# Optimization experiments

Hardware: AMD Instinct MI355X
Metric: run time of the kernel (lower is better)

Reference implementation:

```python
import jax, jax.numpy as jnp
import numpy as np

B, S, D, H = 4, 2048, 1024, 16
DEPTH = D // H


def setup_inputs() -> dict:
    key = jax.random.key(0)
    ks = jax.random.split(key, 12)
    inp = {
        'v': jax.random.normal(ks[0], (B, S, D), dtype=jnp.float32),
        'k': jax.random.normal(ks[1], (B, S, D), dtype=jnp.float32),
        'q': jax.random.normal(ks[2], (B, S, D), dtype=jnp.float32),
        # key-padding mask: 1.0 = masked position, 0.0 = attend
        'mask': jax.random.randint(ks[3], (B, 1, 1, S), 0, 2).astype(jnp.float32),
        'Wq': jax.random.normal(ks[4], (D, D), dtype=jnp.float32) / np.sqrt(D),
        'bq': jnp.zeros((D,), dtype=jnp.float32),
        'Wk': jax.random.normal(ks[5], (D, D), dtype=jnp.float32) / np.sqrt(D),
        'bk': jnp.zeros((D,), dtype=jnp.float32),
        'Wv': jax.random.normal(ks[6], (D, D), dtype=jnp.float32) / np.sqrt(D),
        'bv': jnp.zeros((D,), dtype=jnp.float32),
        'Wo': jax.random.normal(ks[7], (D, D), dtype=jnp.float32) / np.sqrt(D),
        'bo': jnp.zeros((D,), dtype=jnp.float32),
    }
    return inp


def _split_heads(x):
    # [B, S, D] -> [B, H, S, depth]
    b, s, _ = x.shape
    return x.reshape(b, s, H, DEPTH).transpose(0, 2, 1, 3)


def reference(v, k, q, mask, Wq, bq, Wk, bk, Wv, bv, Wo, bo):
    qh = _split_heads(q @ Wq + bq)  # [B,H,S,depth]
    kh = _split_heads(k @ Wk + bk)
    vh = _split_heads(v @ Wv + bv)
    logits = jnp.einsum('bhqd,bhkd->bhqk', qh, kh) / jnp.sqrt(
        jnp.asarray(DEPTH, dtype=qh.dtype))
    logits = logits + mask * (-1e9)
    attn = jax.nn.softmax(logits, axis=-1)  # [B,H,Sq,Sk]
    out = jnp.einsum('bhqk,bhkd->bhqd', attn, vh)
    out = out.transpose(0, 2, 1, 3).reshape(q.shape[0], -1, D)  # [B,S,D]
    return out @ Wo + bo
```

## Files before the change

kernel.cpp:

```cpp
#include <hip/hip_runtime.h>
#include <hip/hip_bf16.h>
#include <stdint.h>


#define S_LEN 2048
#define NHEAD 16
#define DEPTH 64
#define DMODEL 1024

typedef __bf16 bf16x8 __attribute__((ext_vector_type(8)));
typedef float f32x4 __attribute__((ext_vector_type(4)));
typedef uint16_t u16x8 __attribute__((ext_vector_type(8)));
typedef uint16_t u16x4 __attribute__((ext_vector_type(4)));

#if __has_builtin(__builtin_amdgcn_exp2f)
#define EXP2F(x) __builtin_amdgcn_exp2f(x)
#else
#define EXP2F(x) __builtin_exp2f(x)
#endif

__device__ __forceinline__ uint16_t f2bf(float x) {
    __hip_bfloat16 h = __float2bfloat16(x);
    union { __hip_bfloat16 h; uint16_t u; } v; v.h = h; return v.u;
}
__device__ __forceinline__ u16x8 cvt8(const float* p) {
    f32x4 lo = *(const f32x4*)p, hi = *(const f32x4*)(p + 4);
    u16x8 r;
#pragma unroll
    for (int i = 0; i < 4; ++i) { r[i] = f2bf(lo[i]); r[i + 4] = f2bf(hi[i]); }
    return r;
}
__device__ __forceinline__ void async16(const void* g, void* l) {
    __builtin_amdgcn_global_load_lds((__attribute__((address_space(1))) void*)(g),
                                     (__attribute__((address_space(3))) void*)(l),
                                     16, 0, 0);
}

__global__ void mask_scan(const float* __restrict__ mask, int* __restrict__ gidx,
                          int* __restrict__ nb) {
    __shared__ int part[256];
    const int b = blockIdx.x, tid = threadIdx.x;
    int flags[8], cnt = 0;
#pragma unroll
    for (int i = 0; i < 8; ++i) {
        flags[i] = (mask[b * S_LEN + tid * 8 + i] == 0.0f) ? 1 : 0;
        cnt += flags[i];
    }
    part[tid] = cnt;
    __syncthreads();
    for (int st = 1; st < 256; st <<= 1) {
        int v = (tid >= st) ? part[tid - st] : 0;
        __syncthreads();
        part[tid] += v;
        __syncthreads();
    }
    int run = part[tid] - cnt;
#pragma unroll
    for (int i = 0; i < 8; ++i) {
        if (flags[i]) { gidx[b * S_LEN + run] = tid * 8 + i; ++run; }
    }
    if (tid == 255) nb[b] = part[255];
}

__global__ void transpose4(const float* __restrict__ w0, const float* __restrict__ w1,
                           const float* __restrict__ w2, const float* __restrict__ w3,
                           uint16_t* __restrict__ dst) {
    __shared__ uint16_t tile[32][33];
    const float* src = (blockIdx.z == 0) ? w0 : (blockIdx.z == 1) ? w1
                     : (blockIdx.z == 2) ? w2 : w3;
    uint16_t* d = dst + (size_t)blockIdx.z * DMODEL * DMODEL;
    int bx = blockIdx.x * 32, by = blockIdx.y * 32;
    int x = threadIdx.x, y0 = threadIdx.y;
#pragma unroll
    for (int i = 0; i < 4; ++i) {
        int y = y0 + i * 8;
        tile[y][x] = f2bf(src[(size_t)(by + y) * DMODEL + bx + x]);
    }
    __syncthreads();
#pragma unroll
    for (int i = 0; i < 4; ++i) {
        int y = y0 + i * 8;
        d[(size_t)(bx + y) * DMODEL + by + x] = tile[x][y];
    }
}

__global__ void cast2(const float* __restrict__ a, const float* __restrict__ b,
                      uint16_t* __restrict__ da, uint16_t* __restrict__ db) {
    const float* src = blockIdx.y ? b : a;
    uint16_t* dst = blockIdx.y ? db : da;
    size_t i = ((size_t)blockIdx.x * 256 + threadIdx.x) * 8;
    *(u16x8*)(dst + i) = cvt8(src + i);
}

__global__ void zero_tails(const int* __restrict__ nb, uint16_t* __restrict__ Kc,
                           uint16_t* __restrict__ Vc) {
    const int bh = blockIdx.x, b = bh >> 4, t = threadIdx.x;
    const int nbv = nb[b];
    const int end = ((nbv + 63) >> 6) << 6;
    const int tail = end - nbv;
    for (int i = t; i < tail * 64; i += 256) {
        int r = nbv + (i >> 6), c = i & 63;
        Kc[((size_t)bh * S_LEN + r) * DEPTH + c] = 0;
    }
    for (int i = t; i < tail * 64; i += 256) {
        int s = nbv + (i >> 6), d = i & 63;
        int off = s & 63;
        int c1 = ((off & 15) << 2) | (off >> 4);
        int c2 = ((((c1 >> 3) ^ (d & 7)) & 7) << 3) | (c1 & 7);
        Vc[((size_t)bh * DEPTH + d) * S_LEN + (s & ~63) + c2] = 0;
    }
}

__global__ __launch_bounds__(256, 2)
void qkv_gemm(const uint16_t* __restrict__ qb, const uint16_t* __restrict__ kb,
              const float* __restrict__ vf, const uint16_t* __restrict__ WT4,
              const float* __restrict__ bq, const float* __restrict__ bk,
              const float* __restrict__ bv, uint16_t* __restrict__ Qh,
              uint16_t* __restrict__ Kc, uint16_t* __restrict__ Vc,
              const int* __restrict__ gidx, const int* __restrict__ nb, int zbase) {
    const int z = zbase + blockIdx.z;
    const int fid = blockIdx.x + 8 * blockIdx.y;
    const int n0 = ((fid >> 3) & 7) * 128;
    const int m0 = ((((fid >> 6) << 3)) | (fid & 7)) * 128;
    const int b_ = m0 >> 11;
    int nbv = 0x7FFFFFFF;
    if (z >= 1) {
        nbv = nb[b_];
        if ((m0 & 2047) >= nbv) return;
    }

    __shared__ __align__(16) uint16_t As[128 * 32];
    __shared__ __align__(16) uint16_t Bs[128 * 32];

    const int t = threadIdx.x;
    const int lane = t & 63, quad = lane >> 4, l16 = lane & 15;
    const int w = t >> 6, wm = w >> 1, wn = w & 1;
    const int K = DMODEL;

    const int r_ld = lane >> 2;
    const int c_ld = (lane & 3) * 8;
    const uint16_t* gB = WT4 + (size_t)z * DMODEL * DMODEL + (size_t)(n0 + r_ld) * K + c_ld;
    const float* bias = (z == 0) ? bq : (z == 1) ? bk : bv;

    const int srow = t >> 1, scol = (t & 1) * 16;

    const uint16_t* pA0 = nullptr;
    const uint16_t* pA1 = nullptr;
    const float* Af32 = nullptr;
    if (z == 0) {
        pA0 = qb + (size_t)(m0 + (w * 2 + 0) * 16 + r_ld) * K + c_ld;
        pA1 = qb + (size_t)(m0 + (w * 2 + 1) * 16 + r_ld) * K + c_ld;
    } else if (z == 1) {
        int sp0 = (m0 & 2047) + (w * 2 + 0) * 16 + r_ld;
        int sp1 = sp0 + 16;
        int r0 = (sp0 < nbv) ? gidx[(b_ << 11) + sp0] : 0;
        int r1 = (sp1 < nbv) ? gidx[(b_ << 11) + sp1] : 0;
        pA0 = kb + ((size_t)(b_ << 11) + r0) * K + c_ld;
        pA1 = kb + ((size_t)(b_ << 11) + r1) * K + c_ld;
    } else {
        int sp = (m0 & 2047) + srow;
        int rs = (sp < nbv) ? gidx[(b_ << 11) + sp] : 0;
        Af32 = vf + ((size_t)(b_ << 11) + rs) * K + scol;
    }

    f32x4 acc[4][4];
    const f32x4 z4 = {0.f, 0.f, 0.f, 0.f};
#pragma unroll
    for (int mt = 0; mt < 4; ++mt)
#pragma unroll
        for (int nt = 0; nt < 4; ++nt) acc[mt][nt] = z4;

    for (int kc = 0; kc < K; kc += 32) {
#pragma unroll
        for (int i = 0; i < 2; ++i) {
            int c = w * 2 + i;
            async16(gB + (size_t)(c * 16) * K + kc, &Bs[c * 512]);
        }
        if (z <= 1) {
            async16(pA0 + kc, &As[(w * 2 + 0) * 512]);
            async16(pA1 + kc, &As[(w * 2 + 1) * 512]);
        } else {
            *(u16x8*)&As[srow * 32 + scol]     = cvt8(Af32 + kc);
            *(u16x8*)&As[srow * 32 + scol + 8] = cvt8(Af32 + kc + 8);
        }
        __syncthreads();

        bf16x8 af[4], bfr[4];
#pragma unroll
        for (int mt = 0; mt < 4; ++mt)
            af[mt] = *(const bf16x8*)&As[(wm * 64 + mt * 16 + l16) * 32 + quad * 8];
#pragma unroll
        for (int nt = 0; nt < 4; ++nt)
            bfr[nt] = *(const bf16x8*)&Bs[(wn * 64 + nt * 16 + l16) * 32 + quad * 8];
#pragma unroll
        for (int mt = 0; mt < 4; ++mt)
#pragma unroll
            for (int nt = 0; nt < 4; ++nt)
                acc[mt][nt] = __builtin_amdgcn_mfma_f32_16x16x32_bf16(af[mt], bfr[nt],
                                                                      acc[mt][nt], 0, 0, 0);
        __syncthreads();
    }

#pragma unroll
    for (int nt = 0; nt < 4; ++nt) {
        int col = n0 + wn * 64 + nt * 16 + l16;
        float bval = bias[col];
        int h = col >> 6, dp = col & 63;
#pragma unroll
        for (int mt = 0; mt < 4; ++mt) {
#pragma unroll
            for (int r = 0; r < 4; ++r) {
                int row = m0 + wm * 64 + mt * 16 + quad * 4 + r;
                float val = acc[mt][nt][r] + bval;
                int b = row >> 11, s = row & 2047;
                if (z == 0) {
                    Qh[(((size_t)(b * NHEAD + h)) * S_LEN + s) * DEPTH + dp] = f2bf(val);
                } else if (z == 1) {
                    if (s < nbv) {
                        int c2 = ((((dp >> 3) ^ (s & 7)) & 7) << 3) | (dp & 7);
                        Kc[(((size_t)(b * NHEAD + h)) * S_LEN + s) * DEPTH + c2] = f2bf(val);
                    }
                } else {
                    if (s < nbv) {
                        int off = s & 63;
                        int c1 = ((off & 15) << 2) | (off >> 4);
                        int c2 = ((((c1 >> 3) ^ (dp & 7)) & 7) << 3) | (c1 & 7);
                        Vc[(((size_t)(b * NHEAD + h)) * DEPTH + dp) * S_LEN
                           + (s & ~63) + c2] = f2bf(val);
                    }
                }
            }
        }
    }
}

__global__ __launch_bounds__(256, 2)
void out_gemm(const uint16_t* __restrict__ ctx, const uint16_t* __restrict__ Wt,
              const float* __restrict__ bias, float* __restrict__ outp) {
    const int fid = blockIdx.x + 8 * blockIdx.y;
    const int n0 = ((fid >> 3) & 7) * 128;
    const int m0 = ((((fid >> 6) << 3)) | (fid & 7)) * 128;

    __shared__ __align__(16) uint16_t As[128 * 32];
    __shared__ __align__(16) uint16_t Bs[128 * 32];

    const int t = threadIdx.x;
    const int lane = t & 63, quad = lane >> 4, l16 = lane & 15;
    const int w = t >> 6, wm = w >> 1, wn = w & 1;
    const int K = DMODEL;

    const int r_ld = lane >> 2;
    const int c_ld = (lane & 3) * 8;
    const uint16_t* gB = Wt + (size_t)(n0 + r_ld) * K + c_ld;

    int row0 = m0 + (w * 2 + 0) * 16 + r_ld;
    int row1 = row0 + 16;
    const uint16_t* pA0 = ctx + ((size_t)((row0 >> 11) * NHEAD) * S_LEN + (row0 & 2047)) * DEPTH + c_ld;
    const uint16_t* pA1 = ctx + ((size_t)((row1 >> 11) * NHEAD) * S_LEN + (row1 & 2047)) * DEPTH + c_ld;

    f32x4 acc[4][4];
    const f32x4 z4 = {0.f, 0.f, 0.f, 0.f};
#pragma unroll
    for (int mt = 0; mt < 4; ++mt)
#pragma unroll
        for (int nt = 0; nt < 4; ++nt) acc[mt][nt] = z4;

    for (int kc = 0; kc < K; kc += 32) {
#pragma unroll
        for (int i = 0; i < 2; ++i) {
            int c = w * 2 + i;
            async16(gB + (size_t)(c * 16) * K + kc, &Bs[c * 512]);
        }
        size_t aoff = ((size_t)(kc >> 6) << 17) + (kc & 63);
        async16(pA0 + aoff, &As[(w * 2 + 0) * 512]);
        async16(pA1 + aoff, &As[(w * 2 + 1) * 512]);
        __syncthreads();

        bf16x8 af[4], bfr[4];
#pragma unroll
        for (int mt = 0; mt < 4; ++mt)
            af[mt] = *(const bf16x8*)&As[(wm * 64 + mt * 16 + l16) * 32 + quad * 8];
#pragma unroll
        for (int nt = 0; nt < 4; ++nt)
            bfr[nt] = *(const bf16x8*)&Bs[(wn * 64 + nt * 16 + l16) * 32 + quad * 8];
#pragma unroll
        for (int mt = 0; mt < 4; ++mt)
#pragma unroll
            for (int nt = 0; nt < 4; ++nt)
                acc[mt][nt] = __builtin_amdgcn_mfma_f32_16x16x32_bf16(af[mt], bfr[nt],
                                                                      acc[mt][nt], 0, 0, 0);
        __syncthreads();
    }

#pragma unroll
    for (int nt = 0; nt < 4; ++nt) {
        int col = n0 + wn * 64 + nt * 16 + l16;
        float bval = bias[col];
#pragma unroll
        for (int mt = 0; mt < 4; ++mt) {
#pragma unroll
            for (int r = 0; r < 4; ++r) {
                int row = m0 + wm * 64 + mt * 16 + quad * 4 + r;
                outp[(size_t)row * DMODEL + col] = acc[mt][nt][r] + bval;
            }
        }
    }
}

__global__ __launch_bounds__(256, 3)
void flash_attn(const uint16_t* __restrict__ Qh, const uint16_t* __restrict__ Kc,
                const uint16_t* __restrict__ Vc, const int* __restrict__ nb,
                uint16_t* __restrict__ ctx) {
    __shared__ __align__(16) uint16_t Ks[2][64 * 64];
    __shared__ __align__(16) uint16_t Vs[2][64 * 64];
    __shared__ __align__(16) uint16_t Ps[4][16 * 72];

    const int t = threadIdx.x;
    const int w = t >> 6, lane = t & 63, quad = lane >> 4, l16 = lane & 15;
    const int fid = blockIdx.x + 16 * blockIdx.y;
    const int q0 = ((fid >> 3) & 15) * 128;
    const int bh = ((fid >> 7) << 3) | (fid & 7);
    const int b = bh >> 4;
    const int nbv = nb[b];
    const int ntiles = (nbv + 63) >> 6;

    const int srow8 = lane >> 3, scol8 = (lane & 7) * 8;
    const uint16_t* pKn = Kc + ((size_t)bh * S_LEN + w * 16 + srow8) * DEPTH + scol8;
    const uint16_t* pVn = Vc + ((size_t)bh * DEPTH + w * 16 + srow8) * S_LEN + scol8;
    uint16_t* dK0 = &Ks[0][w * 16 * 64];
    uint16_t* dK1 = &Ks[1][w * 16 * 64];
    uint16_t* dV0 = &Vs[0][w * 16 * 64];
    uint16_t* dV1 = &Vs[1][w * 16 * 64];

    bf16x8 aq[2][2];
#pragma unroll
    for (int mt = 0; mt < 2; ++mt)
#pragma unroll
        for (int kc = 0; kc < 2; ++kc)
            aq[mt][kc] = *(const bf16x8*)(Qh + ((size_t)bh * S_LEN + q0 + w * 32 + mt * 16 + l16) * DEPTH
                                          + kc * 32 + quad * 8);

    float lrow[2][4];
    f32x4 Oacc[2][4];
    const f32x4 z4 = {0.f, 0.f, 0.f, 0.f};
#pragma unroll
    for (int mt = 0; mt < 2; ++mt)
#pragma unroll
        for (int r = 0; r < 4; ++r) lrow[mt][r] = 0.f;
#pragma unroll
    for (int mt = 0; mt < 2; ++mt)
#pragma unroll
        for (int nt = 0; nt < 4; ++nt) Oacc[mt][nt] = z4;

    const float C2 = 0.18033688f;
    const float M2 = 17.312340f;
    const int swzk = l16 & 7;

    async16(pKn, dK0); async16(pKn + 8 * DEPTH, dK0 + 8 * 64);
    async16(pVn, dV0); async16(pVn + 8 * S_LEN, dV0 + 8 * 64);
    pKn += 64 * DEPTH; pVn += 64;
    __syncthreads();

    for (int kt = 0; kt < ntiles; ++kt) {
        const int cur = kt & 1;
        if (kt + 1 < ntiles) {
            uint16_t* dK = cur ? dK0 : dK1;
            uint16_t* dV = cur ? dV0 : dV1;
            async16(pKn, dK); async16(pKn + 8 * DEPTH, dK + 8 * 64);
            async16(pVn, dV); async16(pVn + 8 * S_LEN, dV + 8 * 64);
            pKn += 64 * DEPTH; pVn += 64;
        }
        const uint16_t* ksrc = cur ? &Ks[1][0] : &Ks[0][0];
        const uint16_t* vsrc = cur ? &Vs[1][0] : &Vs[0][0];
        const int k0 = kt * 64;

        float pen[4];
#pragma unroll
        for (int nt = 0; nt < 4; ++nt)
            pen[nt] = (k0 + nt * 16 + l16 < nbv) ? -M2 : -2e9f;

        f32x4 sacc[2][4];
#pragma unroll
        for (int mt = 0; mt < 2; ++mt)
#pragma unroll
            for (int nt = 0; nt < 4; ++nt) sacc[mt][nt] = z4;
        __builtin_amdgcn_s_setprio(1);
#pragma unroll
        for (int kc = 0; kc < 2; ++kc) {
#pragma unroll
            for (int nt = 0; nt < 4; ++nt) {
                bf16x8 bk = *(const bf16x8*)&ksrc[(nt * 16 + l16) * 64 + (((kc * 4 + quad) ^ swzk) << 3)];
#pragma unroll
                for (int mt = 0; mt < 2; ++mt)
                    sacc[mt][nt] = __builtin_amdgcn_mfma_f32_16x16x32_bf16(aq[mt][kc], bk,
                                                                           sacc[mt][nt], 0, 0, 0);
            }
        }
        __builtin_amdgcn_s_setprio(0);

        bf16x8 bvr[2][4];
#pragma unroll
        for (int kc = 0; kc < 2; ++kc)
#pragma unroll
            for (int nt = 0; nt < 4; ++nt)
                bvr[kc][nt] = *(const bf16x8*)&vsrc[(nt * 16 + l16) * 64 + (((kc * 4 + quad) ^ swzk) << 3)];

#pragma unroll
        for (int mt = 0; mt < 2; ++mt) {
#pragma unroll
            for (int r = 0; r < 4; ++r) {
                float p0 = EXP2F(fmaf(sacc[mt][0][r], C2, pen[0]));
                float p1 = EXP2F(fmaf(sacc[mt][1][r], C2, pen[1]));
                float p2 = EXP2F(fmaf(sacc[mt][2][r], C2, pen[2]));
                float p3 = EXP2F(fmaf(sacc[mt][3][r], C2, pen[3]));
                lrow[mt][r] += (p0 + p1) + (p2 + p3);
                u16x4 pk;
                pk[0] = f2bf(p0); pk[1] = f2bf(p1); pk[2] = f2bf(p2); pk[3] = f2bf(p3);
                *(u16x4*)&Ps[w][(quad * 4 + r) * 72 + l16 * 4] = pk;
            }
            __builtin_amdgcn_s_setprio(1);
#pragma unroll
            for (int kc = 0; kc < 2; ++kc) {
                bf16x8 ap = *(const bf16x8*)&Ps[w][l16 * 72 + kc * 32 + quad * 8];
#pragma unroll
                for (int nt = 0; nt < 4; ++nt)
                    Oacc[mt][nt] = __builtin_amdgcn_mfma_f32_16x16x32_bf16(ap, bvr[kc][nt],
                                                                           Oacc[mt][nt], 0, 0, 0);
            }
            __builtin_amdgcn_s_setprio(0);
        }
        __syncthreads();
    }

#pragma unroll
    for (int mt = 0; mt < 2; ++mt) {
#pragma unroll
        for (int r = 0; r < 4; ++r) {
            float rs = lrow[mt][r];
            rs += __shfl_xor(rs, 1);
            rs += __shfl_xor(rs, 2);
            rs += __shfl_xor(rs, 4);
            rs += __shfl_xor(rs, 8);
            float inv = 1.0f / rs;
            int srow = q0 + w * 32 + mt * 16 + quad * 4 + r;
            size_t base = ((size_t)bh * S_LEN + srow) * DEPTH;
#pragma unroll
            for (int nt = 0; nt < 4; ++nt)
                ctx[base + nt * 16 + l16] = f2bf(Oacc[mt][nt][r] * inv);
        }
    }
}

extern "C" void kernel_launch(void* const* d_in, const int* in_sizes, int n_in,
                              void* d_out, int out_size, void* d_ws, size_t ws_size,
                              hipStream_t stream) {
    const float* v    = (const float*)d_in[0];
    const float* k    = (const float*)d_in[1];
    const float* q    = (const float*)d_in[2];
    const float* mask = (const float*)d_in[3];
    const float* Wq   = (const float*)d_in[4];
    const float* bq   = (const float*)d_in[5];
    const float* Wk   = (const float*)d_in[6];
    const float* bk   = (const float*)d_in[7];
    const float* Wv   = (const float*)d_in[8];
    const float* bv   = (const float*)d_in[9];
    const float* Wo   = (const float*)d_in[10];
    const float* bo   = (const float*)d_in[11];

    char* p = (char*)d_ws;
    uint16_t* WT4 = (uint16_t*)p; p += (size_t)4 * DMODEL * DMODEL * 2;
    uint16_t* Qh  = (uint16_t*)p; p += (size_t)64 * S_LEN * DEPTH * 2;
    int* gidx     = (int*)p;      p += (size_t)4 * S_LEN * 4;
    int* nb       = (int*)p;      p += 16;
    size_t used = (size_t)(p - (char*)d_ws);
    const size_t kcvc = (size_t)64 * S_LEN * DEPTH * 2;

    uint16_t* qb = (uint16_t*)d_out;
    uint16_t* kb = qb + (size_t)8192 * DMODEL;

    uint16_t *Kc, *Vc;
    const bool bigws = (ws_size >= used + 2 * kcvc);
    if (bigws) { Kc = (uint16_t*)((char*)d_ws + used); Vc = Kc + (size_t)64 * S_LEN * DEPTH; }
    else       { Kc = qb; Vc = kb; }

    mask_scan<<<4, 256, 0, stream>>>(mask, gidx, nb);
    transpose4<<<dim3(32, 32, 4), dim3(32, 8), 0, stream>>>(Wq, Wk, Wv, Wo, WT4);
    cast2<<<dim3(4096, 2), 256, 0, stream>>>(q, k, qb, kb);

    if (bigws) {
        qkv_gemm<<<dim3(8, 64, 3), 256, 0, stream>>>(qb, kb, v, WT4, bq, bk, bv,
                                                     Qh, Kc, Vc, gidx, nb, 0);
    } else {
        qkv_gemm<<<dim3(8, 64, 1), 256, 0, stream>>>(qb, kb, v, WT4, bq, bk, bv,
                                                     Qh, Kc, Vc, gidx, nb, 0);
        qkv_gemm<<<dim3(8, 64, 1), 256, 0, stream>>>(qb, kb, v, WT4, bq, bk, bv,
                                                     Qh, Kc, Vc, gidx, nb, 1);
        qkv_gemm<<<dim3(8, 64, 1), 256, 0, stream>>>(qb, kb, v, WT4, bq, bk, bv,
                                                     Qh, Kc, Vc, gidx, nb, 2);
    }
    zero_tails<<<64, 256, 0, stream>>>(nb, Kc, Vc);

    flash_attn<<<dim3(16, 64), 256, 0, stream>>>(Qh, Kc, Vc, nb, Qh );

    out_gemm<<<dim3(8, 64), 256, 0, stream>>>(Qh, WT4 + (size_t)3 * DMODEL * DMODEL,
                                              bo, (float*)d_out);
}
```

Baseline: 330.0 us.

## Fuse fp32-to-bf16 input cast into QKV GEMM and double-buffer GEMM tiles

Drops the separate cast2 kernel, so the QKV GEMM now loads fp32 q/k directly and converts them to bf16 in registers before writing to LDS. Both the QKV and output GEMMs now use double-buffered LDS, with a software pipeline that prefetches the next K-slice (async B loads plus register-staged A) while the current one is computed. Occupancy hints go from 2 to 3 blocks per SM. Kc/Vc are placed in the output buffer unconditionally, which removes the workspace-size branch. The aim is to cut a memory pass over q/k and hide load latency, at the cost of more LDS and registers and reliance on hand-written waitcnt counts.

```diff
diff --git a/kernel.cpp b/kernel.cpp
--- a/kernel.cpp
+++ b/kernel.cpp
@@ -23,11 +23,10 @@
     __hip_bfloat16 h = __float2bfloat16(x);
     union { __hip_bfloat16 h; uint16_t u; } v; v.h = h; return v.u;
 }
-__device__ __forceinline__ u16x8 cvt8(const float* p) {
-    f32x4 lo = *(const f32x4*)p, hi = *(const f32x4*)(p + 4);
+__device__ __forceinline__ u16x8 pack8(f32x4 a, f32x4 b) {
     u16x8 r;
 #pragma unroll
-    for (int i = 0; i < 4; ++i) { r[i] = f2bf(lo[i]); r[i + 4] = f2bf(hi[i]); }
+    for (int i = 0; i < 4; ++i) { r[i] = f2bf(a[i]); r[i + 4] = f2bf(b[i]); }
     return r;
 }
 __device__ __forceinline__ void async16(const void* g, void* l) {
@@ -84,14 +83,6 @@
     }
 }
 
-__global__ void cast2(const float* __restrict__ a, const float* __restrict__ b,
-                      uint16_t* __restrict__ da, uint16_t* __restrict__ db) {
-    const float* src = blockIdx.y ? b : a;
-    uint16_t* dst = blockIdx.y ? db : da;
-    size_t i = ((size_t)blockIdx.x * 256 + threadIdx.x) * 8;
-    *(u16x8*)(dst + i) = cvt8(src + i);
-}
-
 __global__ void zero_tails(const int* __restrict__ nb, uint16_t* __restrict__ Kc,
                            uint16_t* __restrict__ Vc) {
     const int bh = blockIdx.x, b = bh >> 4, t = threadIdx.x;
@@ -111,14 +102,14 @@
     }
 }
 
-__global__ __launch_bounds__(256, 2)
-void qkv_gemm(const uint16_t* __restrict__ qb, const uint16_t* __restrict__ kb,
+__global__ __launch_bounds__(256, 3)
+void qkv_gemm(const float* __restrict__ qf, const float* __restrict__ kf,
               const float* __restrict__ vf, const uint16_t* __restrict__ WT4,
               const float* __restrict__ bq, const float* __restrict__ bk,
               const float* __restrict__ bv, uint16_t* __restrict__ Qh,
               uint16_t* __restrict__ Kc, uint16_t* __restrict__ Vc,
-              const int* __restrict__ gidx, const int* __restrict__ nb, int zbase) {
-    const int z = zbase + blockIdx.z;
+              const int* __restrict__ gidx, const int* __restrict__ nb) {
+    const int z = blockIdx.z;
     const int fid = blockIdx.x + 8 * blockIdx.y;
     const int n0 = ((fid >> 3) & 7) * 128;
     const int m0 = ((((fid >> 6) << 3)) | (fid & 7)) * 128;
@@ -129,8 +120,8 @@
         if ((m0 & 2047) >= nbv) return;
     }
 
-    __shared__ __align__(16) uint16_t As[128 * 32];
-    __shared__ __align__(16) uint16_t Bs[128 * 32];
+    __shared__ __align__(16) uint16_t As[2][128 * 32];
+    __shared__ __align__(16) uint16_t Bs[2][128 * 32];
 
     const int t = threadIdx.x;
     const int lane = t & 63, quad = lane >> 4, l16 = lane & 15;
@@ -143,24 +134,13 @@
     const float* bias = (z == 0) ? bq : (z == 1) ? bk : bv;
 
     const int srow = t >> 1, scol = (t & 1) * 16;
-
-    const uint16_t* pA0 = nullptr;
-    const uint16_t* pA1 = nullptr;
-    const float* Af32 = nullptr;
+    const float* Af32;
     if (z == 0) {
-        pA0 = qb + (size_t)(m0 + (w * 2 + 0) * 16 + r_ld) * K + c_ld;
-        pA1 = qb + (size_t)(m0 + (w * 2 + 1) * 16 + r_ld) * K + c_ld;
-    } else if (z == 1) {
-        int sp0 = (m0 & 2047) + (w * 2 + 0) * 16 + r_ld;
-        int sp1 = sp0 + 16;
-        int r0 = (sp0 < nbv) ? gidx[(b_ << 11) + sp0] : 0;
-        int r1 = (sp1 < nbv) ? gidx[(b_ << 11) + sp1] : 0;
-        pA0 = kb + ((size_t)(b_ << 11) + r0) * K + c_ld;
-        pA1 = kb + ((size_t)(b_ << 11) + r1) * K + c_ld;
+        Af32 = qf + (size_t)(m0 + srow) * K + scol;
     } else {
         int sp = (m0 & 2047) + srow;
         int rs = (sp < nbv) ? gidx[(b_ << 11) + sp] : 0;
-        Af32 = vf + ((size_t)(b_ << 11) + rs) * K + scol;
+        Af32 = ((z == 1) ? kf : vf) + ((size_t)(b_ << 11) + rs) * K + scol;
     }
 
     f32x4 acc[4][4];
@@ -170,35 +150,67 @@
 #pragma unroll
         for (int nt = 0; nt < 4; ++nt) acc[mt][nt] = z4;
 
-    for (int kc = 0; kc < K; kc += 32) {
+    f32x4 fa[4];
+    auto loadA = [&](int kc) {
+#pragma unroll
+        for (int i = 0; i < 4; ++i) fa[i] = *(const f32x4*)(Af32 + kc + i * 4);
+    };
+    uint16_t* wA0 = &As[0][srow * 32 + scol];
+    uint16_t* wA1 = &As[1][srow * 32 + scol];
+    auto writeA = [&](int buf) {
+        uint16_t* d = buf ? wA1 : wA0;
+        *(u16x8*)d = pack8(fa[0], fa[1]);
+        *(u16x8*)(d + 8) = pack8(fa[2], fa[3]);
+    };
+    auto issueB = [&](int kc, int buf) {
 #pragma unroll
         for (int i = 0; i < 2; ++i) {
             int c = w * 2 + i;
-            async16(gB + (size_t)(c * 16) * K + kc, &Bs[c * 512]);
-        }
-        if (z <= 1) {
-            async16(pA0 + kc, &As[(w * 2 + 0) * 512]);
-            async16(pA1 + kc, &As[(w * 2 + 1) * 512]);
-        } else {
-            *(u16x8*)&As[srow * 32 + scol]     = cvt8(Af32 + kc);
-            *(u16x8*)&As[srow * 32 + scol + 8] = cvt8(Af32 + kc + 8);
-        }
-        __syncthreads();
-
+            async16(gB + (size_t)(c * 16) * K + kc, &Bs[buf][c * 512]);
+        }
+    };
+    auto compute = [&](int buf) {
         bf16x8 af[4], bfr[4];
 #pragma unroll
         for (int mt = 0; mt < 4; ++mt)
-            af[mt] = *(const bf16x8*)&As[(wm * 64 + mt * 16 + l16) * 32 + quad * 8];
+            af[mt] = *(const bf16x8*)&As[buf][(wm * 64 + mt * 16 + l16) * 32 + quad * 8];
 #pragma unroll
         for (int nt = 0; nt < 4; ++nt)
-            bfr[nt] = *(const bf16x8*)&Bs[(wn * 64 + nt * 16 + l16) * 32 + quad * 8];
+            bfr[nt] = *(const bf16x8*)&Bs[buf][(wn * 64 + nt * 16 + l16) * 32 + quad * 8];
 #pragma unroll
         for (int mt = 0; mt < 4; ++mt)
 #pragma unroll
             for (int nt = 0; nt < 4; ++nt)
                 acc[mt][nt] = __builtin_amdgcn_mfma_f32_16x16x32_bf16(af[mt], bfr[nt],
                                                                       acc[mt][nt], 0, 0, 0);
-        __syncthreads();
+    };
+
+    issueB(0, 0);
+    loadA(0);
+    writeA(0);
+    __builtin_amdgcn_sched_barrier(0);
+    loadA(32);
+    asm volatile("s_waitcnt vmcnt(4) lgkmcnt(0)" ::: "memory");
+    __builtin_amdgcn_s_barrier();
+    __builtin_amdgcn_sched_barrier(0);
+
+    for (int s = 0; s < 32; ++s) {
+        const int cb = s & 1;
+        if (s < 31) issueB((s + 1) * 32, cb ^ 1);
+        compute(cb);
+        if (s < 31) {
+            writeA(cb ^ 1);
+            __builtin_amdgcn_sched_barrier(0);
+            if (s < 30) {
+                loadA((s + 2) * 32);
+                __builtin_amdgcn_sched_barrier(0);
+                asm volatile("s_waitcnt vmcnt(4) lgkmcnt(0)" ::: "memory");
+            } else {
+                asm volatile("s_waitcnt vmcnt(0) lgkmcnt(0)" ::: "memory");
+            }
+            __builtin_amdgcn_s_barrier();
+            __builtin_amdgcn_sched_barrier(0);
+        }
     }
 
 #pragma unroll
@@ -234,15 +246,15 @@
     }
 }
 
-__global__ __launch_bounds__(256, 2)
+__global__ __launch_bounds__(256, 3)
 void out_gemm(const uint16_t* __restrict__ ctx, const uint16_t* __restrict__ Wt,
               const float* __restrict__ bias, float* __restrict__ outp) {
     const int fid = blockIdx.x + 8 * blockIdx.y;
     const int n0 = ((fid >> 3) & 7) * 128;
     const int m0 = ((((fid >> 6) << 3)) | (fid & 7)) * 128;
 
-    __shared__ __align__(16) uint16_t As[128 * 32];
-    __shared__ __align__(16) uint16_t Bs[128 * 32];
+    __shared__ __align__(16) uint16_t As[2][128 * 32];
+    __shared__ __align__(16) uint16_t Bs[2][128 * 32];
 
     const int t = threadIdx.x;
     const int lane = t & 63, quad = lane >> 4, l16 = lane & 15;
@@ -258,6 +270,17 @@
     const uint16_t* pA0 = ctx + ((size_t)((row0 >> 11) * NHEAD) * S_LEN + (row0 & 2047)) * DEPTH + c_ld;
     const uint16_t* pA1 = ctx + ((size_t)((row1 >> 11) * NHEAD) * S_LEN + (row1 & 2047)) * DEPTH + c_ld;
 
+    auto stage = [&](int kc, int buf) {
+#pragma unroll
+        for (int i = 0; i < 2; ++i) {
+            int c = w * 2 + i;
+            async16(gB + (size_t)(c * 16) * K + kc, &Bs[buf][c * 512]);
+        }
+        size_t aoff = ((size_t)(kc >> 6) << 17) + (kc & 63);
+        async16(pA0 + aoff, &As[buf][(w * 2 + 0) * 512]);
+        async16(pA1 + aoff, &As[buf][(w * 2 + 1) * 512]);
+    };
+
     f32x4 acc[4][4];
     const f32x4 z4 = {0.f, 0.f, 0.f, 0.f};
 #pragma unroll
@@ -265,31 +288,28 @@
 #pragma unroll
         for (int nt = 0; nt < 4; ++nt) acc[mt][nt] = z4;
 
-    for (int kc = 0; kc < K; kc += 32) {
-#pragma unroll
-        for (int i = 0; i < 2; ++i) {
-            int c = w * 2 + i;
-            async16(gB + (size_t)(c * 16) * K + kc, &Bs[c * 512]);
-        }
-        size_t aoff = ((size_t)(kc >> 6) << 17) + (kc & 63);
-        async16(pA0 + aoff, &As[(w * 2 + 0) * 512]);
-        async16(pA1 + aoff, &As[(w * 2 + 1) * 512]);
-        __syncthreads();
-
-        bf16x8 af[4], bfr[4];
-#pragma unroll
-        for (int mt = 0; mt < 4; ++mt)
-            af[mt] = *(const bf16x8*)&As[(wm * 64 + mt * 16 + l16) * 32 + quad * 8];
-#pragma unroll
-        for (int nt = 0; nt < 4; ++nt)
-            bfr[nt] = *(const bf16x8*)&Bs[(wn * 64 + nt * 16 + l16) * 32 + quad * 8];
-#pragma unroll
-        for (int mt = 0; mt < 4; ++mt)
+    stage(0, 0);
+    __syncthreads();
+
+    for (int s = 0; s < 32; ++s) {
+        const int cb = s & 1;
+        if (s < 31) stage((s + 1) * 32, cb ^ 1);
+        {
+            bf16x8 af[4], bfr[4];
+#pragma unroll
+            for (int mt = 0; mt < 4; ++mt)
+                af[mt] = *(const bf16x8*)&As[cb][(wm * 64 + mt * 16 + l16) * 32 + quad * 8];
 #pragma unroll
             for (int nt = 0; nt < 4; ++nt)
-                acc[mt][nt] = __builtin_amdgcn_mfma_f32_16x16x32_bf16(af[mt], bfr[nt],
-                                                                      acc[mt][nt], 0, 0, 0);
-        __syncthreads();
+                bfr[nt] = *(const bf16x8*)&Bs[cb][(wn * 64 + nt * 16 + l16) * 32 + quad * 8];
+#pragma unroll
+            for (int mt = 0; mt < 4; ++mt)
+#pragma unroll
+                for (int nt = 0; nt < 4; ++nt)
+                    acc[mt][nt] = __builtin_amdgcn_mfma_f32_16x16x32_bf16(af[mt], bfr[nt],
+                                                                          acc[mt][nt], 0, 0, 0);
+        }
+        if (s < 31) __syncthreads();
     }
 
 #pragma unroll
@@ -472,32 +492,15 @@
     uint16_t* Qh  = (uint16_t*)p; p += (size_t)64 * S_LEN * DEPTH * 2;
     int* gidx     = (int*)p;      p += (size_t)4 * S_LEN * 4;
     int* nb       = (int*)p;      p += 16;
-    size_t used = (size_t)(p - (char*)d_ws);
-    const size_t kcvc = (size_t)64 * S_LEN * DEPTH * 2;
-
-    uint16_t* qb = (uint16_t*)d_out;
-    uint16_t* kb = qb + (size_t)8192 * DMODEL;
-
-    uint16_t *Kc, *Vc;
-    const bool bigws = (ws_size >= used + 2 * kcvc);
-    if (bigws) { Kc = (uint16_t*)((char*)d_ws + used); Vc = Kc + (size_t)64 * S_LEN * DEPTH; }
-    else       { Kc = qb; Vc = kb; }
+
+    uint16_t* Kc = (uint16_t*)d_out;
+    uint16_t* Vc = Kc + (size_t)64 * S_LEN * DEPTH;
 
     mask_scan<<<4, 256, 0, stream>>>(mask, gidx, nb);
     transpose4<<<dim3(32, 32, 4), dim3(32, 8), 0, stream>>>(Wq, Wk, Wv, Wo, WT4);
-    cast2<<<dim3(4096, 2), 256, 0, stream>>>(q, k, qb, kb);
-
-    if (bigws) {
-        qkv_gemm<<<dim3(8, 64, 3), 256, 0, stream>>>(qb, kb, v, WT4, bq, bk, bv,
-                                                     Qh, Kc, Vc, gidx, nb, 0);
-    } else {
-        qkv_gemm<<<dim3(8, 64, 1), 256, 0, stream>>>(qb, kb, v, WT4, bq, bk, bv,
-                                                     Qh, Kc, Vc, gidx, nb, 0);
-        qkv_gemm<<<dim3(8, 64, 1), 256, 0, stream>>>(qb, kb, v, WT4, bq, bk, bv,
-                                                     Qh, Kc, Vc, gidx, nb, 1);
-        qkv_gemm<<<dim3(8, 64, 1), 256, 0, stream>>>(qb, kb, v, WT4, bq, bk, bv,
-                                                     Qh, Kc, Vc, gidx, nb, 2);
-    }
+
+    qkv_gemm<<<dim3(8, 64, 3), 256, 0, stream>>>(q, k, v, WT4, bq, bk, bv,
+                                                 Qh, Kc, Vc, gidx, nb);
     zero_tails<<<64, 256, 0, stream>>>(nb, Kc, Vc);
 
     flash_attn<<<dim3(16, 64), 256, 0, stream>>>(Qh, Kc, Vc, nb, Qh );
```

Measured after the change: 330.2 us. No clear change (+0.1%).

## Double-buffer LDS tiles in QKV and output GEMMs with register-prefetched V conversion

Applied to the files above, without the earlier changes.

Both projection GEMMs now use two LDS buffers so the async global-to-LDS loads for the next K-slice are issued before computing the current one, and MFMA sections are wrapped in s_setprio. For the fp32 V input, the next tile is prefetched into registers and converted to bf16 after compute. Launch bounds are raised to three blocks per CU, and the workspace layout is rearranged so Kc/Vc live in the output buffer and the bf16 q/k copies live in the workspace. The aim is to hide global-load latency behind MFMA work, at the cost of doubled LDS use and more register pressure.

```diff
diff --git a/kernel.cpp b/kernel.cpp
--- a/kernel.cpp
+++ b/kernel.cpp
@@ -23,12 +23,15 @@
     __hip_bfloat16 h = __float2bfloat16(x);
     union { __hip_bfloat16 h; uint16_t u; } v; v.h = h; return v.u;
 }
+__device__ __forceinline__ u16x8 pack8(f32x4 a, f32x4 b) {
+    u16x8 r;
+#pragma unroll
+    for (int i = 0; i < 4; ++i) { r[i] = f2bf(a[i]); r[i + 4] = f2bf(b[i]); }
+    return r;
+}
 __device__ __forceinline__ u16x8 cvt8(const float* p) {
     f32x4 lo = *(const f32x4*)p, hi = *(const f32x4*)(p + 4);
-    u16x8 r;
-#pragma unroll
-    for (int i = 0; i < 4; ++i) { r[i] = f2bf(lo[i]); r[i + 4] = f2bf(hi[i]); }
-    return r;
+    return pack8(lo, hi);
 }
 __device__ __forceinline__ void async16(const void* g, void* l) {
     __builtin_amdgcn_global_load_lds((__attribute__((address_space(1))) void*)(g),
@@ -111,7 +114,7 @@
     }
 }
 
-__global__ __launch_bounds__(256, 2)
+__global__ __launch_bounds__(256, 3)
 void qkv_gemm(const uint16_t* __restrict__ qb, const uint16_t* __restrict__ kb,
               const float* __restrict__ vf, const uint16_t* __restrict__ WT4,
               const float* __restrict__ bq, const float* __restrict__ bk,
@@ -129,8 +132,8 @@
         if ((m0 & 2047) >= nbv) return;
     }
 
-    __shared__ __align__(16) uint16_t As[128 * 32];
-    __shared__ __align__(16) uint16_t Bs[128 * 32];
+    __shared__ __align__(16) uint16_t As[2][128 * 32];
+    __shared__ __align__(16) uint16_t Bs[2][128 * 32];
 
     const int t = threadIdx.x;
     const int lane = t & 63, quad = lane >> 4, l16 = lane & 15;
@@ -142,14 +145,13 @@
     const uint16_t* gB = WT4 + (size_t)z * DMODEL * DMODEL + (size_t)(n0 + r_ld) * K + c_ld;
     const float* bias = (z == 0) ? bq : (z == 1) ? bk : bv;
 
-    const int srow = t >> 1, scol = (t & 1) * 16;
-
     const uint16_t* pA0 = nullptr;
     const uint16_t* pA1 = nullptr;
-    const float* Af32 = nullptr;
+    const float* pAa = nullptr;
+    const float* pAb = nullptr;
     if (z == 0) {
         pA0 = qb + (size_t)(m0 + (w * 2 + 0) * 16 + r_ld) * K + c_ld;
-        pA1 = qb + (size_t)(m0 + (w * 2 + 1) * 16 + r_ld) * K + c_ld;
+        pA1 = pA0 + (size_t)16 * K;
     } else if (z == 1) {
         int sp0 = (m0 & 2047) + (w * 2 + 0) * 16 + r_ld;
         int sp1 = sp0 + 16;
@@ -158,9 +160,12 @@
         pA0 = kb + ((size_t)(b_ << 11) + r0) * K + c_ld;
         pA1 = kb + ((size_t)(b_ << 11) + r1) * K + c_ld;
     } else {
-        int sp = (m0 & 2047) + srow;
-        int rs = (sp < nbv) ? gidx[(b_ << 11) + sp] : 0;
-        Af32 = vf + ((size_t)(b_ << 11) + rs) * K + scol;
+        int spa = (m0 & 2047) + (t >> 2);
+        int spb = spa + 64;
+        int ra = (spa < nbv) ? gidx[(b_ << 11) + spa] : 0;
+        int rb = (spb < nbv) ? gidx[(b_ << 11) + spb] : 0;
+        pAa = vf + ((size_t)(b_ << 11) + ra) * K + (t & 3) * 8;
+        pAb = vf + ((size_t)(b_ << 11) + rb) * K + (t & 3) * 8;
     }
 
     f32x4 acc[4][4];
@@ -170,36 +175,67 @@
 #pragma unroll
         for (int nt = 0; nt < 4; ++nt) acc[mt][nt] = z4;
 
-    for (int kc = 0; kc < K; kc += 32) {
-#pragma unroll
-        for (int i = 0; i < 2; ++i) {
-            int c = w * 2 + i;
-            async16(gB + (size_t)(c * 16) * K + kc, &Bs[c * 512]);
-        }
-        if (z <= 1) {
-            async16(pA0 + kc, &As[(w * 2 + 0) * 512]);
-            async16(pA1 + kc, &As[(w * 2 + 1) * 512]);
-        } else {
-            *(u16x8*)&As[srow * 32 + scol]     = cvt8(Af32 + kc);
-            *(u16x8*)&As[srow * 32 + scol + 8] = cvt8(Af32 + kc + 8);
-        }
+    f32x4 frA[4], frB[4];
+
+#define STAGEB(KC, BUF) do {                                                   \
+        async16(gB + (size_t)((w * 2 + 0) * 16) * K + (KC), &Bs[(BUF)][(w * 2 + 0) * 512]); \
+        async16(gB + (size_t)((w * 2 + 1) * 16) * K + (KC), &Bs[(BUF)][(w * 2 + 1) * 512]); \
+    } while (0)
+#define STAGEA(KC, BUF) do {                                                   \
+        async16(pA0 + (KC), &As[(BUF)][(w * 2 + 0) * 512]);                    \
+        async16(pA1 + (KC), &As[(BUF)][(w * 2 + 1) * 512]);                    \
+    } while (0)
+#define LOADA2(KC, FR) do {                                                    \
+        FR[0] = *(const f32x4*)(pAa + (KC));                                   \
+        FR[1] = *(const f32x4*)(pAa + (KC) + 4);                               \
+        FR[2] = *(const f32x4*)(pAb + (KC));                                   \
+        FR[3] = *(const f32x4*)(pAb + (KC) + 4);                               \
+    } while (0)
+#define WRITEA2(BUF, FR) do {                                                  \
+        uint16_t* d_ = &As[(BUF)][0] + t * 8;                                  \
+        *(u16x8*)d_ = pack8(FR[0], FR[1]);                                     \
+        *(u16x8*)(d_ + 2048) = pack8(FR[2], FR[3]);                            \
+    } while (0)
+#define COMPUTE(BUF) do {                                                      \
+        bf16x8 af[4], bfr[4];                                                  \
+        _Pragma("unroll")                                                      \
+        for (int mt = 0; mt < 4; ++mt)                                         \
+            af[mt] = *(const bf16x8*)&As[(BUF)][(wm * 64 + mt * 16 + l16) * 32 + quad * 8]; \
+        _Pragma("unroll")                                                      \
+        for (int nt = 0; nt < 4; ++nt)                                         \
+            bfr[nt] = *(const bf16x8*)&Bs[(BUF)][(wn * 64 + nt * 16 + l16) * 32 + quad * 8]; \
+        __builtin_amdgcn_s_setprio(1);                                         \
+        _Pragma("unroll")                                                      \
+        for (int mt = 0; mt < 4; ++mt)                                         \
+            _Pragma("unroll")                                                  \
+            for (int nt = 0; nt < 4; ++nt)                                     \
+                acc[mt][nt] = __builtin_amdgcn_mfma_f32_16x16x32_bf16(af[mt], bfr[nt], \
+                                                                      acc[mt][nt], 0, 0, 0); \
+        __builtin_amdgcn_s_setprio(0);                                         \
+    } while (0)
+
+    STAGEB(0, 0);
+    if (z <= 1) { STAGEA(0, 0); }
+    else { LOADA2(0, frA); WRITEA2(0, frA); LOADA2(32, frA); }
+    __syncthreads();
+
+    for (int s = 0; s < 32; s += 2) {
+        if (s + 1 < 32) { STAGEB((s + 1) * 32, 1); if (z <= 1) STAGEA((s + 1) * 32, 1); }
+        if (z == 2 && s + 2 < 32) LOADA2((s + 2) * 32, frB);
+        COMPUTE(0);
+        if (z == 2 && s + 1 < 32) WRITEA2(1, frA);
         __syncthreads();
-
-        bf16x8 af[4], bfr[4];
-#pragma unroll
-        for (int mt = 0; mt < 4; ++mt)
-            af[mt] = *(const bf16x8*)&As[(wm * 64 + mt * 16 + l16) * 32 + quad * 8];
-#pragma unroll
-        for (int nt = 0; nt < 4; ++nt)
-            bfr[nt] = *(const bf16x8*)&Bs[(wn * 64 + nt * 16 + l16) * 32 + quad * 8];
-#pragma unroll
-        for (int mt = 0; mt < 4; ++mt)
-#pragma unroll
-            for (int nt = 0; nt < 4; ++nt)
-                acc[mt][nt] = __builtin_amdgcn_mfma_f32_16x16x32_bf16(af[mt], bfr[nt],
-                                                                      acc[mt][nt], 0, 0, 0);
+        if (s + 2 < 32) { STAGEB((s + 2) * 32, 0); if (z <= 1) STAGEA((s + 2) * 32, 0); }
+        if (z == 2 && s + 3 < 32) LOADA2((s + 3) * 32, frA);
+        COMPUTE(1);
+        if (z == 2 && s + 2 < 32) WRITEA2(0, frB);
         __syncthreads();
     }
+#undef STAGEB
+#undef STAGEA
+#undef LOADA2
+#undef WRITEA2
+#undef COMPUTE
 
 #pragma unroll
     for (int nt = 0; nt < 4; ++nt) {
@@ -234,15 +270,15 @@
     }
 }
 
-__global__ __launch_bounds__(256, 2)
+__global__ __launch_bounds__(256, 3)
 void out_gemm(const uint16_t* __restrict__ ctx, const uint16_t* __restrict__ Wt,
               const float* __restrict__ bias, float* __restrict__ outp) {
     const int fid = blockIdx.x + 8 * blockIdx.y;
     const int n0 = ((fid >> 3) & 7) * 128;
     const int m0 = ((((fid >> 6) << 3)) | (fid & 7)) * 128;
 
-    __shared__ __align__(16) uint16_t As[128 * 32];
-    __shared__ __align__(16) uint16_t Bs[128 * 32];
+    __shared__ __align__(16) uint16_t As[2][128 * 32];
+    __shared__ __align__(16) uint16_t Bs[2][128 * 32];
 
     const int t = threadIdx.x;
     const int lane = t & 63, quad = lane >> 4, l16 = lane & 15;
@@ -258,6 +294,14 @@
     const uint16_t* pA0 = ctx + ((size_t)((row0 >> 11) * NHEAD) * S_LEN + (row0 & 2047)) * DEPTH + c_ld;
     const uint16_t* pA1 = ctx + ((size_t)((row1 >> 11) * NHEAD) * S_LEN + (row1 & 2047)) * DEPTH + c_ld;
 
+    auto stage = [&](int kc, int buf) {
+        async16(gB + (size_t)((w * 2 + 0) * 16) * K + kc, &Bs[buf][(w * 2 + 0) * 512]);
+        async16(gB + (size_t)((w * 2 + 1) * 16) * K + kc, &Bs[buf][(w * 2 + 1) * 512]);
+        size_t aoff = ((size_t)(kc >> 6) << 17) + (kc & 63);
+        async16(pA0 + aoff, &As[buf][(w * 2 + 0) * 512]);
+        async16(pA1 + aoff, &As[buf][(w * 2 + 1) * 512]);
+    };
+
     f32x4 acc[4][4];
     const f32x4 z4 = {0.f, 0.f, 0.f, 0.f};
 #pragma unroll
@@ -265,30 +309,29 @@
 #pragma unroll
         for (int nt = 0; nt < 4; ++nt) acc[mt][nt] = z4;
 
-    for (int kc = 0; kc < K; kc += 32) {
-#pragma unroll
-        for (int i = 0; i < 2; ++i) {
-            int c = w * 2 + i;
-            async16(gB + (size_t)(c * 16) * K + kc, &Bs[c * 512]);
-        }
-        size_t aoff = ((size_t)(kc >> 6) << 17) + (kc & 63);
-        async16(pA0 + aoff, &As[(w * 2 + 0) * 512]);
-        async16(pA1 + aoff, &As[(w * 2 + 1) * 512]);
-        __syncthreads();
-
-        bf16x8 af[4], bfr[4];
-#pragma unroll
-        for (int mt = 0; mt < 4; ++mt)
-            af[mt] = *(const bf16x8*)&As[(wm * 64 + mt * 16 + l16) * 32 + quad * 8];
-#pragma unroll
-        for (int nt = 0; nt < 4; ++nt)
-            bfr[nt] = *(const bf16x8*)&Bs[(wn * 64 + nt * 16 + l16) * 32 + quad * 8];
-#pragma unroll
-        for (int mt = 0; mt < 4; ++mt)
+    stage(0, 0);
+    __syncthreads();
+
+    for (int s = 0; s < 32; ++s) {
+        const int cb = s & 1;
+        if (s + 1 < 32) stage((s + 1) * 32, cb ^ 1);
+        {
+            bf16x8 af[4], bfr[4];
+#pragma unroll
+            for (int mt = 0; mt < 4; ++mt)
+                af[mt] = *(const bf16x8*)&As[cb][(wm * 64 + mt * 16 + l16) * 32 + quad * 8];
 #pragma unroll
             for (int nt = 0; nt < 4; ++nt)
-                acc[mt][nt] = __builtin_amdgcn_mfma_f32_16x16x32_bf16(af[mt], bfr[nt],
-                                                                      acc[mt][nt], 0, 0, 0);
+                bfr[nt] = *(const bf16x8*)&Bs[cb][(wn * 64 + nt * 16 + l16) * 32 + quad * 8];
+            __builtin_amdgcn_s_setprio(1);
+#pragma unroll
+            for (int mt = 0; mt < 4; ++mt)
+#pragma unroll
+                for (int nt = 0; nt < 4; ++nt)
+                    acc[mt][nt] = __builtin_amdgcn_mfma_f32_16x16x32_bf16(af[mt], bfr[nt],
+                                                                          acc[mt][nt], 0, 0, 0);
+            __builtin_amdgcn_s_setprio(0);
+        }
         __syncthreads();
     }
 
@@ -473,15 +516,21 @@
     int* gidx     = (int*)p;      p += (size_t)4 * S_LEN * 4;
     int* nb       = (int*)p;      p += 16;
     size_t used = (size_t)(p - (char*)d_ws);
-    const size_t kcvc = (size_t)64 * S_LEN * DEPTH * 2;
-
-    uint16_t* qb = (uint16_t*)d_out;
-    uint16_t* kb = qb + (size_t)8192 * DMODEL;
-
-    uint16_t *Kc, *Vc;
-    const bool bigws = (ws_size >= used + 2 * kcvc);
-    if (bigws) { Kc = (uint16_t*)((char*)d_ws + used); Vc = Kc + (size_t)64 * S_LEN * DEPTH; }
-    else       { Kc = qb; Vc = kb; }
+    const size_t half16 = (size_t)8192 * DMODEL * 2;
+
+    const bool bigws = (ws_size >= used + 2 * half16);
+    uint16_t *qb, *kb, *Kc, *Vc;
+    if (bigws) {
+        qb = (uint16_t*)((char*)d_ws + used);
+        kb = qb + (size_t)8192 * DMODEL;
+        Kc = (uint16_t*)d_out;
+        Vc = Kc + (size_t)64 * S_LEN * DEPTH;
+    } else {
+        qb = (uint16_t*)d_out;
+        kb = qb + (size_t)8192 * DMODEL;
+        Kc = qb;
+        Vc = kb;
+    }
 
     mask_scan<<<4, 256, 0, stream>>>(mask, gidx, nb);
     transpose4<<<dim3(32, 32, 4), dim3(32, 8), 0, stream>>>(Wq, Wk, Wv, Wo, WT4);
```

Measured after the change: 335.3 us. No clear change (+1.6%).
